# Optimization experiments

Hardware: AMD Instinct MI355X
Metric: run time of the kernel (lower is better)

Reference implementation:

```python
import jax, jax.numpy as jnp
import numpy as np

SIGMA_XY = 15.0
SIGMA_RGB = 0.125
B, C, H, W = 1, 1, 96, 96


def setup_inputs() -> dict:
    key = jax.random.key(0)
    k1, k2 = jax.random.split(key)
    inp = jax.random.uniform(k1, (B, C, H, W), dtype=jnp.float32)   # segmentation probs in [0,1]
    img = jax.random.uniform(k2, (B, 3, H, W), dtype=jnp.float32)   # RGB in [0,1]
    return {"input": inp, "image": img}


def _crf_loss_single(s, img, pos):
    # s: [C, N] probs, img: [3, N] colors, pos: [N, 2] scaled xy coords
    feat = jnp.concatenate([pos, img.T / SIGMA_RGB], axis=1)        # [N, 5] joint bilateral features
    sq = jnp.sum(feat * feat, axis=1)                                # [N]
    d2 = sq[:, None] + sq[None, :] - 2.0 * (feat @ feat.T)           # [N, N] squared feature distance
    Wm = jnp.exp(-0.5 * jnp.maximum(d2, 0.0))                        # [N, N] Gaussian bilateral affinity
    # dense CRF relaxed Potts loss: sum_c s_c^T W (1 - s_c)
    return jnp.sum((Wm @ (1.0 - s.T)) * s.T)


def reference(input, image):
    b, c, h, w = input.shape
    n = h * w
    yy, xx = jnp.meshgrid(jnp.arange(h, dtype=input.dtype),
                          jnp.arange(w, dtype=input.dtype), indexing="ij")
    pos = jnp.stack([xx, yy], axis=-1).reshape(n, 2) / SIGMA_XY      # [N, 2]
    s = input.reshape(b, c, n)
    img = image.reshape(b, 3, n)
    losses = jax.vmap(lambda sv, iv: _crf_loss_single(sv, iv, pos))(s, img)
    return jnp.sum(losses) / n                                        # per-pixel normalized scalar loss
```

## Files before the change

kernel.cpp:

```cpp
#include <hip/hip_runtime.h>

#define NPTS 9216
#define WIDTH 96
#define TILE 256
#define NTILES 36

__global__ __launch_bounds__(256)
void crf_feat_kernel(const float* __restrict__ s,
                     const float* __restrict__ img,
                     float* __restrict__ feat,
                     float* __restrict__ out) {
    int p = blockIdx.x * 256 + threadIdx.x;
    if (p == 0) out[0] = 0.0f;
    if (p >= NPTS) return;
    int y = p / WIDTH;
    int x = p - y * WIDTH;
    float sv = s[p];
    float4 a, b;
    a.x = (float)x * (1.0f / 15.0f);
    a.y = (float)y * (1.0f / 15.0f);
    a.z = img[p]          * 8.0f;
    a.w = img[NPTS + p]   * 8.0f;
    b.x = img[2*NPTS + p] * 8.0f;
    b.y = 1.0f - sv;
    b.z = sv;
    b.w = 0.0f;
    float4* f4 = (float4*)feat;
    f4[2*p]     = a;
    f4[2*p + 1] = b;
}

__global__ __launch_bounds__(256)
void crf_pair_kernel(const float* __restrict__ feat,
                     float* __restrict__ out) {
    __shared__ float sh[TILE * 8];
    __shared__ float wavesum[4];

    const int tid = threadIdx.x;
    const int i = blockIdx.x * TILE + tid;
    const int jbase = blockIdx.y * TILE;

    const float4* f4 = (const float4*)feat;
    float4 ja = f4[2*(jbase + tid)];
    float4 jb = f4[2*(jbase + tid) + 1];
    ((float4*)sh)[2*tid]     = ja;
    ((float4*)sh)[2*tid + 1] = jb;

    float4 fa = f4[2*i];
    float4 fb = f4[2*i + 1];
    const float si = fb.z;

    __syncthreads();

    float acc = 0.0f;
    #pragma unroll 8
    for (int j = 0; j < TILE; ++j) {
        const float* p = &sh[8*j];
        float dx = fa.x - p[0];
        float dy = fa.y - p[1];
        float dr = fa.z - p[2];
        float dg = fa.w - p[3];
        float db = fb.x - p[4];
        float d2 = dx*dx;
        d2 = fmaf(dy, dy, d2);
        d2 = fmaf(dr, dr, d2);
        d2 = fmaf(dg, dg, d2);
        d2 = fmaf(db, db, d2);
        float w = __expf(-0.5f * d2);
        acc = fmaf(w, p[5], acc);
    }
    acc *= si;

    #pragma unroll
    for (int off = 32; off > 0; off >>= 1)
        acc += __shfl_down(acc, off, 64);
    if ((tid & 63) == 0) wavesum[tid >> 6] = acc;
    __syncthreads();
    if (tid == 0) {
        float t = wavesum[0] + wavesum[1] + wavesum[2] + wavesum[3];
        atomicAdd(out, t * (1.0f / (float)NPTS));
    }
}

extern "C" void kernel_launch(void* const* d_in, const int* in_sizes, int n_in,
                              void* d_out, int out_size, void* d_ws, size_t ws_size,
                              hipStream_t stream) {
    const float* s   = (const float*)d_in[0];
    const float* img = (const float*)d_in[1];
    float* out  = (float*)d_out;
    float* feat = (float*)d_ws;

    crf_feat_kernel<<<NTILES, 256, 0, stream>>>(s, img, feat, out);
    dim3 grid(NTILES, NTILES);
    crf_pair_kernel<<<grid, 256, 0, stream>>>(feat, out);
}
```

Before: 88.65 us.

## Expand squared distance into dot products with fp16 fdot2 and exp2

Rewrites the pairwise Gaussian as exp2 of a bias plus dot products. Features are prescaled by sqrt(log2 e) and packed as fp16 pairs so each pair needs three fdot2 instructions and one exp2. The per-j log(1-s) is folded into the exponent to remove the multiply. Each thread now handles four i points against a 128-wide j tile, reusing shared-memory loads across more work. The fp16 features and the expanded form can lose precision, and log(1-s) becomes -inf when s is exactly 1.

```diff
diff --git a/kernel.cpp b/kernel.cpp
--- a/kernel.cpp
+++ b/kernel.cpp
@@ -1,14 +1,23 @@
 #include <hip/hip_runtime.h>
 
-#define NPTS 9216
+#define NPTS  9216
 #define WIDTH 96
-#define TILE 256
-#define NTILES 36
+#define IPT   4
+#define IBLK  (256*IPT)
+#define NIB   9
+#define JTILE 128
+#define NJB   72
+
+#define KSCALE 1.2011224087864498f
+
+typedef _Float16 half2v __attribute__((ext_vector_type(2)));
+union H2F { half2v h; float f; };
 
 __global__ __launch_bounds__(256)
 void crf_feat_kernel(const float* __restrict__ s,
                      const float* __restrict__ img,
-                     float* __restrict__ feat,
+                     float4* __restrict__ arrJ,
+                     float4* __restrict__ arrI,
                      float* __restrict__ out) {
     int p = blockIdx.x * 256 + threadIdx.x;
     if (p == 0) out[0] = 0.0f;
@@ -16,69 +25,89 @@
     int y = p / WIDTH;
     int x = p - y * WIDTH;
     float sv = s[p];
-    float4 a, b;
-    a.x = (float)x * (1.0f / 15.0f);
-    a.y = (float)y * (1.0f / 15.0f);
-    a.z = img[p]          * 8.0f;
-    a.w = img[NPTS + p]   * 8.0f;
-    b.x = img[2*NPTS + p] * 8.0f;
-    b.y = 1.0f - sv;
-    b.z = sv;
-    b.w = 0.0f;
-    float4* f4 = (float4*)feat;
-    f4[2*p]     = a;
-    f4[2*p + 1] = b;
+    float xs = (float)x * (KSCALE / 15.0f);
+    float ys = (float)y * (KSCALE / 15.0f);
+    float rs = img[p]          * (8.0f * KSCALE);
+    float gs = img[NPTS + p]   * (8.0f * KSCALE);
+    float bs = img[2*NPTS + p] * (8.0f * KSCALE);
+    _Float16 xh = (_Float16)xs, yh = (_Float16)ys;
+    _Float16 rh = (_Float16)rs, gh = (_Float16)gs, bh = (_Float16)bs;
+    float xr = (float)xh, yr = (float)yh, rr = (float)rh, gr = (float)gh, br = (float)bh;
+    float hs = -0.5f * (xr*xr + yr*yr + rr*rr + gr*gr + br*br);
+    float hsl = hs + __builtin_amdgcn_logf(1.0f - sv);
+
+    H2F xy; xy.h = half2v{xh, yh};
+    H2F rg; rg.h = half2v{rh, gh};
+    H2F b0; b0.h = half2v{bh, (_Float16)0.0f};
+
+    float4 rj, ri;
+    rj.x = xy.f; rj.y = rg.f; rj.z = b0.f; rj.w = hsl;
+    ri.x = xy.f; ri.y = rg.f; ri.z = b0.f; ri.w = hs;
+    arrJ[p] = rj;
+    arrI[p] = ri;
 }
 
 __global__ __launch_bounds__(256)
-void crf_pair_kernel(const float* __restrict__ feat,
+void crf_pair_kernel(const float4* __restrict__ arrJ,
+                     const float4* __restrict__ arrI,
+                     const float* __restrict__ s,
                      float* __restrict__ out) {
-    __shared__ float sh[TILE * 8];
+    __shared__ float4 shJ[JTILE];
     __shared__ float wavesum[4];
 
-    const int tid = threadIdx.x;
-    const int i = blockIdx.x * TILE + tid;
-    const int jbase = blockIdx.y * TILE;
+    const int tid   = threadIdx.x;
+    const int ibase = blockIdx.x * IBLK;
+    const int jbase = blockIdx.y * JTILE;
 
-    const float4* f4 = (const float4*)feat;
-    float4 ja = f4[2*(jbase + tid)];
-    float4 jb = f4[2*(jbase + tid) + 1];
-    ((float4*)sh)[2*tid]     = ja;
-    ((float4*)sh)[2*tid + 1] = jb;
+    if (tid < JTILE) shJ[tid] = arrJ[jbase + tid];
 
-    float4 fa = f4[2*i];
-    float4 fb = f4[2*i + 1];
-    const float si = fb.z;
+    half2v xyi[IPT], rgi[IPT], b0i[IPT];
+    float  hsi[IPT], svi[IPT];
+    #pragma unroll
+    for (int k = 0; k < IPT; ++k) {
+        int i = ibase + k * 256 + tid;
+        float4 r = arrI[i];
+        H2F a; a.f = r.x; xyi[k] = a.h;
+        H2F b; b.f = r.y; rgi[k] = b.h;
+        H2F c; c.f = r.z; b0i[k] = c.h;
+        hsi[k] = r.w;
+        svi[k] = s[i];
+    }
 
     __syncthreads();
 
-    float acc = 0.0f;
-    #pragma unroll 8
-    for (int j = 0; j < TILE; ++j) {
-        const float* p = &sh[8*j];
-        float dx = fa.x - p[0];
-        float dy = fa.y - p[1];
-        float dr = fa.z - p[2];
-        float dg = fa.w - p[3];
-        float db = fb.x - p[4];
-        float d2 = dx*dx;
-        d2 = fmaf(dy, dy, d2);
-        d2 = fmaf(dr, dr, d2);
-        d2 = fmaf(dg, dg, d2);
-        d2 = fmaf(db, db, d2);
-        float w = __expf(-0.5f * d2);
-        acc = fmaf(w, p[5], acc);
+    float acc[IPT];
+    #pragma unroll
+    for (int k = 0; k < IPT; ++k) acc[k] = 0.0f;
+
+    #pragma unroll 4
+    for (int j = 0; j < JTILE; ++j) {
+        float4 rj = shJ[j];
+        H2F a; a.f = rj.x;
+        H2F b; b.f = rj.y;
+        H2F c; c.f = rj.z;
+        const half2v xyj = a.h, rgj = b.h, b0j = c.h;
+        const float hslj = rj.w;
+        #pragma unroll
+        for (int k = 0; k < IPT; ++k) {
+            float e = hsi[k] + hslj;
+            e = __builtin_amdgcn_fdot2(xyi[k], xyj, e, false);
+            e = __builtin_amdgcn_fdot2(rgi[k], rgj, e, false);
+            e = __builtin_amdgcn_fdot2(b0i[k], b0j, e, false);
+            acc[k] += __builtin_amdgcn_exp2f(e);
+        }
     }
-    acc *= si;
+
+    float t = acc[0]*svi[0] + acc[1]*svi[1] + acc[2]*svi[2] + acc[3]*svi[3];
 
     #pragma unroll
     for (int off = 32; off > 0; off >>= 1)
-        acc += __shfl_down(acc, off, 64);
-    if ((tid & 63) == 0) wavesum[tid >> 6] = acc;
+        t += __shfl_down(t, off, 64);
+    if ((tid & 63) == 0) wavesum[tid >> 6] = t;
     __syncthreads();
     if (tid == 0) {
-        float t = wavesum[0] + wavesum[1] + wavesum[2] + wavesum[3];
-        atomicAdd(out, t * (1.0f / (float)NPTS));
+        float r = wavesum[0] + wavesum[1] + wavesum[2] + wavesum[3];
+        atomicAdd(out, r * (1.0f / (float)NPTS));
     }
 }
 
@@ -87,10 +116,12 @@
                               hipStream_t stream) {
     const float* s   = (const float*)d_in[0];
     const float* img = (const float*)d_in[1];
-    float* out  = (float*)d_out;
-    float* feat = (float*)d_ws;
+    float* out = (float*)d_out;
 
-    crf_feat_kernel<<<NTILES, 256, 0, stream>>>(s, img, feat, out);
-    dim3 grid(NTILES, NTILES);
-    crf_pair_kernel<<<grid, 256, 0, stream>>>(feat, out);
+    float4* arrJ = (float4*)d_ws;
+    float4* arrI = arrJ + NPTS;
+
+    crf_feat_kernel<<<NPTS/256, 256, 0, stream>>>(s, img, arrJ, arrI, out);
+    dim3 grid(NIB, NJB);
+    crf_pair_kernel<<<grid, 256, 0, stream>>>(arrJ, arrI, s, out);
 }
```

New measurement: 78.13 us. -11.9%, faster.
